# Performance work log

Hardware: AMD Instinct MI355X
Metric: run time of the kernel (lower is better)

Reference implementation:

```python
import jax, jax.numpy as jnp
import numpy as np

G, N, E, F = 1000, 256, 1024, 128
D1, D2, K1, K2 = 128, 64, 32, 8
MACRO_D, LABELS, ME = 128, 10, 16000


def gcn_conv(x, src, dst, W, b):
    """PyG GCNConv: add self-loops, symmetric deg normalization, XW aggregate."""
    n = x.shape[0]
    loop = jnp.arange(n)
    s = jnp.concatenate([src, loop])
    d = jnp.concatenate([dst, loop])
    deg = jax.ops.segment_sum(jnp.ones_like(s, dtype=x.dtype), d, num_segments=n)
    dinv = jax.lax.rsqrt(jnp.maximum(deg, 1e-12))  # deg >= 1 due to self-loops
    norm = dinv[s] * dinv[d]                        # [E+n]
    xw = x @ W                                      # [n, out]
    msg = xw[s] * norm[:, None]
    return jax.ops.segment_sum(msg, d, num_segments=n) + b


def setup_inputs() -> dict:
    key = jax.random.key(0)
    ks = jax.random.split(key, 12)
    g = lambda k, shp, fan: (jax.random.normal(k, shp, jnp.float32) / np.sqrt(fan)).astype(jnp.float32)
    return {
        "graph_features": jax.random.normal(ks[0], (G, N, F), jnp.float32),
        "graph_edges": jax.random.randint(ks[1], (G, 2, E), 0, N),
        "macro_edges": jax.random.randint(ks[2], (2, ME), 0, G),
        "W1": g(ks[3], (F, D1), F), "b1": jnp.zeros((D1,), jnp.float32),
        "W2": g(ks[4], (D1, D2), D1), "b2": jnp.zeros((D2,), jnp.float32),
        "Wf1": g(ks[5], (D2, K1), D2), "bf1": jnp.zeros((K1,), jnp.float32),
        "Wf2": g(ks[6], (K1, K2), K1), "bf2": jnp.zeros((K2,), jnp.float32),
        "Wm1": g(ks[7], (D2 * K2, MACRO_D), D2 * K2), "bm1": jnp.zeros((MACRO_D,), jnp.float32),
        "Wm2": g(ks[8], (MACRO_D, LABELS), MACRO_D), "bm2": jnp.zeros((LABELS,), jnp.float32),
    }


def reference(graph_features, graph_edges, macro_edges,
              W1, b1, W2, b2, Wf1, bf1, Wf2, bf2, Wm1, bm1, Wm2, bm2):
    def sage(x, edges):
        src, dst = edges[0], edges[1]
        h1 = jax.nn.relu(gcn_conv(x, src, dst, W1, b1))      # [N, D1]
        h2 = gcn_conv(h1, src, dst, W2, b2)                  # [N, D2]
        a = jnp.tanh(h2 @ Wf1 + bf1)                         # [N, K1]
        att = jax.nn.softmax(a @ Wf2 + bf2, axis=0)          # softmax over nodes, [N, K2]
        emb = (att.T @ h2).reshape(-1)                       # [K2*D2]
        P = att.T @ att - jnp.eye(K2, dtype=x.dtype)         # [K2, K2]
        pen = jnp.sum(jnp.sqrt(jnp.sum(P * P, axis=1)))      # sum of row L2 norms
        return emb, pen

    embs, pens = jax.vmap(sage)(graph_features, graph_edges)  # [G, K2*D2], [G]
    penalty = jnp.mean(pens)

    msrc, mdst = macro_edges[0], macro_edges[1]
    h = jax.nn.relu(gcn_conv(embs, msrc, mdst, Wm1, bm1))     # [G, MACRO_D]
    logits = gcn_conv(h, msrc, mdst, Wm2, bm2)                # [G, LABELS]
    predictions = jax.nn.log_softmax(logits, axis=1)
    return predictions, penalty
```

## Files before the change

kernel.cpp:

```cpp
#include <hip/hip_runtime.h>
#include <math.h>

typedef __attribute__((ext_vector_type(8))) short short8;
typedef __attribute__((ext_vector_type(4))) float f32x4;

#define G_ 1000
#define N_ 256
#define E_ 1024
#define F_ 128
#define D1_ 128
#define D2_ 64
#define K1_ 32
#define K2_ 8
#define MD_ 128
#define LB_ 10
#define ME_ 16000

#define OFS_PEN    0
#define OFS_EMB    16
#define OFS_XW1M   512016
#define OFS_XW2M   640016
#define OFS_DINVM  650016
#define OFS_WNORM  651016
#define OFS_ROWSTM 667016
#define OFS_WSRC   668032
#define OFS_WFRAG  676032

static __device__ __forceinline__ unsigned short f2bf(float f) {
  unsigned u = __builtin_bit_cast(unsigned, f);
  u += 0x7fff + ((u >> 16) & 1);
  return (unsigned short)(u >> 16);
}
static __device__ __forceinline__ float bf2f(unsigned short h) {
  return __builtin_bit_cast(float, (unsigned)h << 16);
}

__global__ __launch_bounds__(256)
void prep_kernel(const float* __restrict__ W1, const float* __restrict__ W2,
                 const float* __restrict__ Wf1,
                 unsigned short* __restrict__ frag, float* __restrict__ ws) {
  int t = blockIdx.x * 256 + threadIdx.x;
  if (t == 0) ws[OFS_PEN] = 0.f;
  unsigned short* w1f  = frag;
  unsigned short* w2f  = frag + 16384;
  unsigned short* wf1h = frag + 24576;
  unsigned short* wf1l = frag + 26624;
  for (int idx = t; idx < 16384; idx += gridDim.x * 256) {
    int j = idx & 7, l = (idx >> 3) & 63, ks = (idx >> 9) & 3, nt = idx >> 11;
    w1f[idx] = f2bf(W1[(ks * 32 + (l >> 4) * 8 + j) * D1_ + nt * 16 + (l & 15)]);
  }
  for (int idx = t; idx < 8192; idx += gridDim.x * 256) {
    int j = idx & 7, l = (idx >> 3) & 63, ks = (idx >> 9) & 3, nt = idx >> 11;
    w2f[idx] = f2bf(W2[(ks * 32 + (l >> 4) * 8 + j) * D2_ + nt * 16 + (l & 15)]);
  }
  for (int idx = t; idx < 2048; idx += gridDim.x * 256) {
    int j = idx & 7, l = (idx >> 3) & 63, ks = (idx >> 9) & 1, nt = idx >> 10;
    float v = Wf1[(ks * 32 + (l >> 4) * 8 + j) * K1_ + nt * 16 + (l & 15)];
    unsigned short hi = f2bf(v);
    wf1h[idx] = hi;
    wf1l[idx] = f2bf(v - bf2f(hi));
  }
}

__global__ __launch_bounds__(512, 4)
void graph_kernel(const float* __restrict__ X, const int* __restrict__ GE,
                  const unsigned short* __restrict__ FR,
                  const float* __restrict__ b1, const float* __restrict__ b2,
                  const float* __restrict__ bf1, const float* __restrict__ bf2,
                  const float* __restrict__ Wf2,
                  float* __restrict__ ws)
{
  const unsigned short* W1F  = FR;
  const unsigned short* W2F  = FR + 16384;
  const unsigned short* Wf1H = FR + 24576;
  const unsigned short* Wf1L = FR + 26624;

  extern __shared__ unsigned char smemraw[];
  unsigned short* chunkA = (unsigned short*)smemraw;
  unsigned short* h2T    = (unsigned short*)smemraw;
  unsigned short* h2s  = (unsigned short*)(smemraw + 33792);
  float*          a_stf = (float*)(smemraw + 33792);
  float*          enorm  = (float*)(smemraw + 70656);
  unsigned short* att_hi = (unsigned short*)(smemraw + 70656);
  unsigned short* att_lo = (unsigned short*)(smemraw + 74880);
  unsigned short* esrc   = (unsigned short*)(smemraw + 74752);
  int*            rowst  = (int*)(smemraw + 76800);
  int*            fill   = (int*)(smemraw + 77824);
  float*          dinv_s = (float*)(smemraw + 78848);
  float*          red    = (float*)(smemraw + 79872);

  const int g = blockIdx.x, tid = threadIdx.x;
  const int w = tid >> 6, lane = tid & 63;
  const int l15 = lane & 15, l4 = lane >> 4;
  const float* xg = X + (size_t)g * (N_ * F_);
  const int*   esG = GE + (size_t)g * (2 * E_);

  if (tid < 256) fill[tid] = 0;
  __syncthreads();
  int s0 = esG[tid * 2], d0 = esG[E_ + tid * 2];
  int s1 = esG[tid * 2 + 1], d1 = esG[E_ + tid * 2 + 1];
  atomicAdd(&fill[d0], 1);
  atomicAdd(&fill[d1], 1);
  __syncthreads();
  int myrow = 0;
  if (tid < 256) {
    int deg = fill[tid];
    dinv_s[tid] = rsqrtf((float)deg + 1.f);
    int v = deg;
#pragma unroll
    for (int off = 1; off < 64; off <<= 1) {
      int u = __shfl_up(v, off);
      if (lane >= off) v += u;
    }
    if (lane == 63) ((int*)red)[w] = v;
    myrow = v - deg;
  }
  __syncthreads();
  if (tid < 256) {
    int pre = 0;
#pragma unroll
    for (int q = 0; q < 4; ++q) if (q < w) pre += ((int*)red)[q];
    rowst[tid] = myrow + pre;
    fill[tid] = 0;
  }
  __syncthreads();
  {
    int pos = rowst[d0] + atomicAdd(&fill[d0], 1);
    esrc[pos] = (unsigned short)s0;
    enorm[pos] = dinv_s[s0] * dinv_s[d0];
    pos = rowst[d1] + atomicAdd(&fill[d1], 1);
    esrc[pos] = (unsigned short)s1;
    enorm[pos] = dinv_s[s1] * dinv_s[d1];
  }
  __syncthreads();

  const int nd = tid >> 1, jhalf = tid & 1;
  const int rb = rowst[nd], rc = fill[nd];
  const float dii = dinv_s[nd] * dinv_s[nd];

  short8 xA[2][4];
#pragma unroll
  for (int mt = 0; mt < 2; ++mt) {
    const float* xr = xg + (w * 32 + mt * 16 + l15) * F_ + l4 * 8;
#pragma unroll
    for (int ks = 0; ks < 4; ++ks) {
      float4 u = *(const float4*)(xr + ks * 32);
      float4 v2 = *(const float4*)(xr + ks * 32 + 4);
      short8 t;
      t[0] = (short)f2bf(u.x);  t[1] = (short)f2bf(u.y);
      t[2] = (short)f2bf(u.z);  t[3] = (short)f2bf(u.w);
      t[4] = (short)f2bf(v2.x); t[5] = (short)f2bf(v2.y);
      t[6] = (short)f2bf(v2.z); t[7] = (short)f2bf(v2.w);
      xA[mt][ks] = t;
    }
  }

  f32x4 acc2[2][4];
#pragma unroll
  for (int mt = 0; mt < 2; ++mt)
#pragma unroll
    for (int nt = 0; nt < 4; ++nt) acc2[mt][nt] = (f32x4){0.f, 0.f, 0.f, 0.f};

  for (int c = 0; c < 4; ++c) {
    __syncthreads();
    f32x4 acc1[2][2];
#pragma unroll
    for (int mt = 0; mt < 2; ++mt) { acc1[mt][0] = (f32x4){0.f,0.f,0.f,0.f}; acc1[mt][1] = (f32x4){0.f,0.f,0.f,0.f}; }
#pragma unroll
    for (int ks = 0; ks < 4; ++ks) {
      short8 bA = *(const short8*)(W1F + (((2 * c + 0) * 4 + ks) * 64 + lane) * 8);
      short8 bB = *(const short8*)(W1F + (((2 * c + 1) * 4 + ks) * 64 + lane) * 8);
#pragma unroll
      for (int mt = 0; mt < 2; ++mt) {
        acc1[mt][0] = __builtin_amdgcn_mfma_f32_16x16x32_bf16(xA[mt][ks], bA, acc1[mt][0], 0, 0, 0);
        acc1[mt][1] = __builtin_amdgcn_mfma_f32_16x16x32_bf16(xA[mt][ks], bB, acc1[mt][1], 0, 0, 0);
      }
    }
#pragma unroll
    for (int mt = 0; mt < 2; ++mt)
#pragma unroll
      for (int ntl = 0; ntl < 2; ++ntl)
#pragma unroll
        for (int r = 0; r < 4; ++r)
          chunkA[(w * 32 + mt * 16 + l4 * 4 + r) * 40 + ntl * 16 + l15] = f2bf(acc1[mt][ntl][r]);
    __syncthreads();
    float gacc[16];
    {
      const unsigned short* rp = chunkA + nd * 40 + jhalf * 16;
      short8 v0 = *(const short8*)(rp);
      short8 v1 = *(const short8*)(rp + 8);
#pragma unroll
      for (int j = 0; j < 8; ++j) {
        gacc[j]     = dii * bf2f((unsigned short)v0[j]);
        gacc[8 + j] = dii * bf2f((unsigned short)v1[j]);
      }
    }
    for (int e = 0; e < rc; ++e) {
      int s = esrc[rb + e]; float nm = enorm[rb + e];
      const unsigned short* sp = chunkA + s * 40 + jhalf * 16;
      short8 v0 = *(const short8*)(sp);
      short8 v1 = *(const short8*)(sp + 8);
#pragma unroll
      for (int j = 0; j < 8; ++j) {
        gacc[j]     = fmaf(nm, bf2f((unsigned short)v0[j]), gacc[j]);
        gacc[8 + j] = fmaf(nm, bf2f((unsigned short)v1[j]), gacc[8 + j]);
      }
    }
    const float* bp = b1 + c * 32 + jhalf * 16;
    __syncthreads();
    {
      short8 o0, o1;
#pragma unroll
      for (int j = 0; j < 8; ++j) {
        o0[j] = (short)f2bf(fmaxf(gacc[j] + bp[j], 0.f));
        o1[j] = (short)f2bf(fmaxf(gacc[8 + j] + bp[8 + j], 0.f));
      }
      *(short8*)(chunkA + nd * 40 + jhalf * 16) = o0;
      *(short8*)(chunkA + nd * 40 + jhalf * 16 + 8) = o1;
    }
    __syncthreads();
    {
      short8 hA0 = *(const short8*)(chunkA + (w * 32 + 0 * 16 + l15) * 40 + l4 * 8);
      short8 hA1 = *(const short8*)(chunkA + (w * 32 + 1 * 16 + l15) * 40 + l4 * 8);
#pragma unroll
      for (int nt = 0; nt < 4; ++nt) {
        short8 bf = *(const short8*)(W2F + ((nt * 4 + c) * 64 + lane) * 8);
        acc2[0][nt] = __builtin_amdgcn_mfma_f32_16x16x32_bf16(hA0, bf, acc2[0][nt], 0, 0, 0);
        acc2[1][nt] = __builtin_amdgcn_mfma_f32_16x16x32_bf16(hA1, bf, acc2[1][nt], 0, 0, 0);
      }
    }
  }

#pragma unroll
  for (int mt = 0; mt < 2; ++mt)
#pragma unroll
    for (int nt = 0; nt < 4; ++nt)
#pragma unroll
      for (int r = 0; r < 4; ++r)
        h2s[(w * 32 + mt * 16 + l4 * 4 + r) * 72 + nt * 16 + l15] = f2bf(acc2[mt][nt][r]);
  __syncthreads();
  float g2[32];
  {
    const unsigned short* rp = h2s + nd * 72 + jhalf * 32;
#pragma unroll
    for (int q = 0; q < 4; ++q) {
      short8 v = *(const short8*)(rp + q * 8);
#pragma unroll
      for (int j = 0; j < 8; ++j) g2[q * 8 + j] = dii * bf2f((unsigned short)v[j]);
    }
  }
  for (int e = 0; e < rc; ++e) {
    int s = esrc[rb + e]; float nm = enorm[rb + e];
    const unsigned short* sp = h2s + s * 72 + jhalf * 32;
#pragma unroll
    for (int q = 0; q < 4; ++q) {
      short8 v = *(const short8*)(sp + q * 8);
#pragma unroll
      for (int j = 0; j < 8; ++j) g2[q * 8 + j] = fmaf(nm, bf2f((unsigned short)v[j]), g2[q * 8 + j]);
    }
  }
  const float* b2p = b2 + jhalf * 32;
  __syncthreads();
  {
#pragma unroll
    for (int q = 0; q < 4; ++q) {
      short8 o;
#pragma unroll
      for (int j = 0; j < 8; ++j) o[j] = (short)f2bf(g2[q * 8 + j] + b2p[q * 8 + j]);
      *(short8*)(h2s + nd * 72 + jhalf * 32 + q * 8) = o;
    }
#pragma unroll
    for (int i = 0; i < 32; ++i)
      h2T[(jhalf * 32 + i) * 264 + nd] = f2bf(g2[i] + b2p[i]);
  }
  __syncthreads();

  short8 hA[2][2];
#pragma unroll
  for (int mt = 0; mt < 2; ++mt)
#pragma unroll
    for (int ks = 0; ks < 2; ++ks)
      hA[mt][ks] = *(const short8*)(h2s + (w * 32 + mt * 16 + l15) * 72 + ks * 32 + l4 * 8);
  f32x4 aacc[2][2];
#pragma unroll
  for (int mt = 0; mt < 2; ++mt) { aacc[mt][0] = (f32x4){0.f,0.f,0.f,0.f}; aacc[mt][1] = (f32x4){0.f,0.f,0.f,0.f}; }
#pragma unroll
  for (int ks = 0; ks < 2; ++ks)
#pragma unroll
    for (int nt = 0; nt < 2; ++nt) {
      short8 bh = *(const short8*)(Wf1H + ((nt * 2 + ks) * 64 + lane) * 8);
      short8 bl = *(const short8*)(Wf1L + ((nt * 2 + ks) * 64 + lane) * 8);
#pragma unroll
      for (int mt = 0; mt < 2; ++mt) {
        aacc[mt][nt] = __builtin_amdgcn_mfma_f32_16x16x32_bf16(hA[mt][ks], bh, aacc[mt][nt], 0, 0, 0);
        aacc[mt][nt] = __builtin_amdgcn_mfma_f32_16x16x32_bf16(hA[mt][ks], bl, aacc[mt][nt], 0, 0, 0);
      }
    }
  __syncthreads();
#pragma unroll
  for (int mt = 0; mt < 2; ++mt)
#pragma unroll
    for (int nt = 0; nt < 2; ++nt)
#pragma unroll
      for (int r = 0; r < 4; ++r)
        a_stf[(w * 32 + mt * 16 + l4 * 4 + r) * 34 + nt * 16 + l15] =
            tanhf(aacc[mt][nt][r] + bf1[nt * 16 + l15]);
  __syncthreads();

  float lv[8], ex[8];
  if (tid < 256) {
#pragma unroll
    for (int jj = 0; jj < 8; ++jj) lv[jj] = bf2[jj];
    const float* ar = a_stf + tid * 34;
    for (int j = 0; j < 32; ++j) {
      float av = ar[j];
      const float* wr = Wf2 + j * K2_;
#pragma unroll
      for (int jj = 0; jj < 8; ++jj) lv[jj] = fmaf(av, wr[jj], lv[jj]);
    }
    float mx[8];
#pragma unroll
    for (int jj = 0; jj < 8; ++jj) mx[jj] = lv[jj];
#pragma unroll
    for (int off = 1; off < 64; off <<= 1)
#pragma unroll
      for (int jj = 0; jj < 8; ++jj) mx[jj] = fmaxf(mx[jj], __shfl_xor(mx[jj], off));
    if (lane == 0)
#pragma unroll
      for (int jj = 0; jj < 8; ++jj) red[w * 8 + jj] = mx[jj];
  }
  __syncthreads();
  if (tid < 256) {
#pragma unroll
    for (int jj = 0; jj < 8; ++jj) {
      float m = fmaxf(fmaxf(red[jj], red[8 + jj]), fmaxf(red[16 + jj], red[24 + jj]));
      ex[jj] = expf(lv[jj] - m);
    }
    float sm[8];
#pragma unroll
    for (int jj = 0; jj < 8; ++jj) sm[jj] = ex[jj];
#pragma unroll
    for (int off = 1; off < 64; off <<= 1)
#pragma unroll
      for (int jj = 0; jj < 8; ++jj) sm[jj] += __shfl_xor(sm[jj], off);
    if (lane == 0)
#pragma unroll
      for (int jj = 0; jj < 8; ++jj) red[32 + w * 8 + jj] = sm[jj];
  }
  __syncthreads();
  if (tid < 256) {
#pragma unroll
    for (int jj = 0; jj < 8; ++jj) {
      float tot = red[32 + jj] + red[40 + jj] + red[48 + jj] + red[56 + jj];
      float av = ex[jj] / tot;
      unsigned short hi = f2bf(av);
      att_hi[jj * 264 + tid] = hi;
      att_lo[jj * 264 + tid] = f2bf(av - bf2f(hi));
    }
  }
  __syncthreads();

  const int rl = l15 & 7;
  if (w < 4) {
    f32x4 d = (f32x4){0.f, 0.f, 0.f, 0.f};
#pragma unroll
    for (int ks = 0; ks < 8; ++ks) {
      short8 ah = *(const short8*)(att_hi + rl * 264 + ks * 32 + l4 * 8);
      short8 al = *(const short8*)(att_lo + rl * 264 + ks * 32 + l4 * 8);
      short8 bv = *(const short8*)(h2T + (w * 16 + l15) * 264 + ks * 32 + l4 * 8);
      d = __builtin_amdgcn_mfma_f32_16x16x32_bf16(ah, bv, d, 0, 0, 0);
      d = __builtin_amdgcn_mfma_f32_16x16x32_bf16(al, bv, d, 0, 0, 0);
    }
    if (l4 < 2) {
      float* eg = ws + OFS_EMB + (size_t)g * 512;
#pragma unroll
      for (int r = 0; r < 4; ++r)
        eg[(l4 * 4 + r) * 64 + w * 16 + l15] = d[r];
    }
  } else if (w == 4) {
    f32x4 p = (f32x4){0.f, 0.f, 0.f, 0.f};
#pragma unroll
    for (int ks = 0; ks < 8; ++ks) {
      short8 ah = *(const short8*)(att_hi + rl * 264 + ks * 32 + l4 * 8);
      short8 al = *(const short8*)(att_lo + rl * 264 + ks * 32 + l4 * 8);
      p = __builtin_amdgcn_mfma_f32_16x16x32_bf16(ah, ah, p, 0, 0, 0);
      p = __builtin_amdgcn_mfma_f32_16x16x32_bf16(ah, al, p, 0, 0, 0);
      p = __builtin_amdgcn_mfma_f32_16x16x32_bf16(al, ah, p, 0, 0, 0);
    }
    if (l4 < 2 && l15 < 8) {
#pragma unroll
      for (int r = 0; r < 4; ++r) {
        float v = p[r];
        if (l4 * 4 + r == l15) v -= 1.f;
        red[64 + (l4 * 4 + r) * 8 + l15] = v * v;
      }
    }
  }
  __syncthreads();
  if (tid < 8) {
    float s2 = 0.f;
#pragma unroll
    for (int k = 0; k < 8; ++k) s2 += red[64 + tid * 8 + k];
    red[128 + tid] = sqrtf(s2);
  }
  __syncthreads();
  if (tid == 0) {
    float p = 0.f;
#pragma unroll
    for (int k = 0; k < 8; ++k) p += red[128 + k];
    atomicAdd(&ws[OFS_PEN], p);
  }
}

__global__ __launch_bounds__(1024)
void macro_csr(const int* __restrict__ me, float* __restrict__ ws) {
  __shared__ int cnt[1000];
  __shared__ float dinvL[1000];
  __shared__ int wtot[16];
  int t = threadIdx.x, lane = t & 63, wv = t >> 6;
  for (int i = t; i < 1000; i += 1024) cnt[i] = 0;
  __syncthreads();
  for (int e = t; e < ME_; e += 1024) atomicAdd(&cnt[me[ME_ + e]], 1);
  __syncthreads();
  int v = (t < 1000) ? cnt[t] : 0;
  float di = rsqrtf((float)v + 1.f);
  if (t < 1000) { dinvL[t] = di; ws[OFS_DINVM + t] = di; }
  int sc = v;
#pragma unroll
  for (int off = 1; off < 64; off <<= 1) {
    int u = __shfl_up(sc, off);
    if (lane >= off) sc += u;
  }
  if (lane == 63) wtot[wv] = sc;
  __syncthreads();
  int pre = 0;
#pragma unroll
  for (int q = 0; q < 16; ++q) if (q < wv) pre += wtot[q];
  int rs = pre + sc - v;
  int* rowstM = (int*)(ws + OFS_ROWSTM);
  if (t < 1000) rowstM[t] = rs;
  if (t == 0) rowstM[1000] = ME_;
  __syncthreads();
  if (t < 1000) cnt[t] = rs;
  __syncthreads();
  unsigned short* wsrc = (unsigned short*)(ws + OFS_WSRC);
  for (int e = t; e < ME_; e += 1024) {
    int s = me[e], d = me[ME_ + e];
    int pos = atomicAdd(&cnt[d], 1);
    wsrc[pos] = (unsigned short)s;
    ws[OFS_WNORM + pos] = dinvL[s] * dinvL[d];
  }
}

__global__ __launch_bounds__(128)
void macro1(const float* __restrict__ Wm1, float* __restrict__ ws) {
  __shared__ float er[512];
  int g = blockIdx.x, t = threadIdx.x;
  *(float4*)&er[t * 4] = *(const float4*)&ws[OFS_EMB + (size_t)g * 512 + t * 4];
  __syncthreads();
  float acc = 0.f;
#pragma unroll 4
  for (int k = 0; k < 512; ++k) acc = fmaf(er[k], Wm1[k * MD_ + t], acc);
  ws[OFS_XW1M + g * MD_ + t] = acc;
}

__global__ __launch_bounds__(128)
void macro2(const float* __restrict__ bm1, const float* __restrict__ Wm2, float* __restrict__ ws) {
  __shared__ float wred[2][10];
  int g = blockIdx.x, t = threadIdx.x;
  const int* rowstM = (const int*)(ws + OFS_ROWSTM);
  const unsigned short* wsrc = (const unsigned short*)(ws + OFS_WSRC);
  int e0 = rowstM[g], e1 = rowstM[g + 1];
  float di = ws[OFS_DINVM + g];
  float acc = di * di * ws[OFS_XW1M + g * MD_ + t];
  for (int e = e0; e < e1; ++e)
    acc = fmaf(ws[OFS_WNORM + e], ws[OFS_XW1M + (int)wsrc[e] * MD_ + t], acc);
  float hv = fmaxf(acc + bm1[t], 0.f);
  float part[10];
#pragma unroll
  for (int j = 0; j < 10; ++j) part[j] = hv * Wm2[t * LB_ + j];
#pragma unroll
  for (int off = 1; off < 64; off <<= 1)
#pragma unroll
    for (int j = 0; j < 10; ++j) part[j] += __shfl_xor(part[j], off);
  if ((t & 63) == 0)
#pragma unroll
    for (int j = 0; j < 10; ++j) wred[t >> 6][j] = part[j];
  __syncthreads();
  if (t < 10) ws[OFS_XW2M + g * LB_ + t] = wred[0][t] + wred[1][t];
}

__global__ __launch_bounds__(64)
void macro3(const float* __restrict__ bm2, const float* __restrict__ ws, float* __restrict__ out) {
  int g = blockIdx.x, t = threadIdx.x;
  const int* rowstM = (const int*)(ws + OFS_ROWSTM);
  const unsigned short* wsrc = (const unsigned short*)(ws + OFS_WSRC);
  int e0 = rowstM[g], e1 = rowstM[g + 1];
  float di = ws[OFS_DINVM + g];
  float lg = -1e30f;
  if (t < 10) {
    float acc = di * di * ws[OFS_XW2M + g * LB_ + t];
    for (int e = e0; e < e1; ++e)
      acc = fmaf(ws[OFS_WNORM + e], ws[OFS_XW2M + (int)wsrc[e] * LB_ + t], acc);
    lg = acc + bm2[t];
  }
  float m = lg;
#pragma unroll
  for (int off = 1; off < 16; off <<= 1) m = fmaxf(m, __shfl_xor(m, off));
  float e_ = (t < 10) ? expf(lg - m) : 0.f;
  float s = e_;
#pragma unroll
  for (int off = 1; off < 16; off <<= 1) s += __shfl_xor(s, off);
  if (t < 10) out[g * LB_ + t] = lg - m - logf(s);
  if (g == 0 && t == 63) out[10000] = ws[OFS_PEN] * 0.001f;
}

extern "C" void kernel_launch(void* const* d_in, const int* in_sizes, int n_in,
                              void* d_out, int out_size, void* d_ws, size_t ws_size,
                              hipStream_t stream)
{
  const float* X   = (const float*)d_in[0];
  const int*   GE  = (const int*)d_in[1];
  const int*   MEe = (const int*)d_in[2];
  const float* W1  = (const float*)d_in[3];
  const float* b1  = (const float*)d_in[4];
  const float* W2  = (const float*)d_in[5];
  const float* b2  = (const float*)d_in[6];
  const float* Wf1 = (const float*)d_in[7];
  const float* bf1 = (const float*)d_in[8];
  const float* Wf2 = (const float*)d_in[9];
  const float* bf2 = (const float*)d_in[10];
  const float* Wm1 = (const float*)d_in[11];
  const float* bm1 = (const float*)d_in[12];
  const float* Wm2 = (const float*)d_in[13];
  const float* bm2 = (const float*)d_in[14];
  float* ws  = (float*)d_ws;
  float* out = (float*)d_out;

  unsigned short* frag = (unsigned short*)(ws + OFS_WFRAG);

  prep_kernel<<<32, 256, 0, stream>>>(W1, W2, Wf1, frag, ws);
  macro_csr<<<1, 1024, 0, stream>>>(MEe, ws);

  size_t lds = 80896;
  graph_kernel<<<G_, 512, lds, stream>>>(X, GE, frag, b1, b2, bf1, bf2, Wf2, ws);

  macro1<<<G_, 128, 0, stream>>>(Wm1, ws);
  macro2<<<G_, 128, 0, stream>>>(bm1, Wm2, ws);
  macro3<<<G_, 64, 0, stream>>>(bm2, ws, out);
}
```

Baseline: 417.6 us.

## Process layer-1 in two 64-wide chunks with prefetched edges and shared staging

Layer 1 of the per-graph GCN now runs in two 64-column chunks instead of four 32-column chunks. This halves the number of barrier-separated gather passes over the CSR neighbour lists and widens each gather row to 32 values per thread. The first four edge sources and norms are preloaded into registers and reused by both the layer-1 and layer-2 aggregations. The staging buffer is unified and h2T is moved to its own region. f2bf now uses the library bf16 conversion, and the extra register pressure (32-float accumulators, wider acc1) may lower occupancy.

After: 457.7 us. +9.6%, slower.

```diff
diff --git a/kernel.cpp b/kernel.cpp
--- a/kernel.cpp
+++ b/kernel.cpp
@@ -1,4 +1,5 @@
 #include <hip/hip_runtime.h>
+#include <hip/hip_bf16.h>
 #include <math.h>
 
 typedef __attribute__((ext_vector_type(8))) short short8;
@@ -27,9 +28,7 @@
 #define OFS_WFRAG  676032
 
 static __device__ __forceinline__ unsigned short f2bf(float f) {
-  unsigned u = __builtin_bit_cast(unsigned, f);
-  u += 0x7fff + ((u >> 16) & 1);
-  return (unsigned short)(u >> 16);
+  return __builtin_bit_cast(unsigned short, __float2bfloat16(f));
 }
 static __device__ __forceinline__ float bf2f(unsigned short h) {
   return __builtin_bit_cast(float, (unsigned)h << 16);
@@ -76,10 +75,9 @@
   const unsigned short* Wf1L = FR + 26624;
 
   extern __shared__ unsigned char smemraw[];
-  unsigned short* chunkA = (unsigned short*)smemraw;
-  unsigned short* h2T    = (unsigned short*)smemraw;
-  unsigned short* h2s  = (unsigned short*)(smemraw + 33792);
-  float*          a_stf = (float*)(smemraw + 33792);
+  unsigned short* STG   = (unsigned short*)smemraw;
+  float*          a_stf = (float*)smemraw;
+  unsigned short* h2T   = (unsigned short*)(smemraw + 36864);
   float*          enorm  = (float*)(smemraw + 70656);
   unsigned short* att_hi = (unsigned short*)(smemraw + 70656);
   unsigned short* att_lo = (unsigned short*)(smemraw + 74880);
@@ -135,8 +133,16 @@
   __syncthreads();
 
   const int nd = tid >> 1, jhalf = tid & 1;
+  const int jh32 = jhalf * 32;
   const int rb = rowst[nd], rc = fill[nd];
   const float dii = dinv_s[nd] * dinv_s[nd];
+
+  int   es0 = nd, es1 = nd, es2 = nd, es3 = nd;
+  float en0 = 0.f, en1 = 0.f, en2 = 0.f, en3 = 0.f;
+  if (rc > 0) { es0 = esrc[rb];     en0 = enorm[rb]; }
+  if (rc > 1) { es1 = esrc[rb + 1]; en1 = enorm[rb + 1]; }
+  if (rc > 2) { es2 = esrc[rb + 2]; en2 = enorm[rb + 2]; }
+  if (rc > 3) { es3 = esrc[rb + 3]; en3 = enorm[rb + 3]; }
 
   short8 xA[2][4];
 #pragma unroll
@@ -161,117 +167,140 @@
 #pragma unroll
     for (int nt = 0; nt < 4; ++nt) acc2[mt][nt] = (f32x4){0.f, 0.f, 0.f, 0.f};
 
-  for (int c = 0; c < 4; ++c) {
+#define GATHER32(SRC, NM)                                                      \
+  {                                                                            \
+    const unsigned short* sp = STG + (SRC) * 72 + jh32;                        \
+    short8 v0 = *(const short8*)(sp);                                          \
+    short8 v1 = *(const short8*)(sp + 8);                                      \
+    short8 v2_ = *(const short8*)(sp + 16);                                    \
+    short8 v3 = *(const short8*)(sp + 24);                                     \
+    _Pragma("unroll")                                                          \
+    for (int j = 0; j < 8; ++j) {                                              \
+      gacc[j]      = fmaf((NM), bf2f((unsigned short)v0[j]), gacc[j]);         \
+      gacc[8 + j]  = fmaf((NM), bf2f((unsigned short)v1[j]), gacc[8 + j]);     \
+      gacc[16 + j] = fmaf((NM), bf2f((unsigned short)v2_[j]), gacc[16 + j]);   \
+      gacc[24 + j] = fmaf((NM), bf2f((unsigned short)v3[j]), gacc[24 + j]);    \
+    }                                                                          \
+  }
+
+  for (int c = 0; c < 2; ++c) {
     __syncthreads();
-    f32x4 acc1[2][2];
-#pragma unroll
-    for (int mt = 0; mt < 2; ++mt) { acc1[mt][0] = (f32x4){0.f,0.f,0.f,0.f}; acc1[mt][1] = (f32x4){0.f,0.f,0.f,0.f}; }
-#pragma unroll
-    for (int ks = 0; ks < 4; ++ks) {
-      short8 bA = *(const short8*)(W1F + (((2 * c + 0) * 4 + ks) * 64 + lane) * 8);
-      short8 bB = *(const short8*)(W1F + (((2 * c + 1) * 4 + ks) * 64 + lane) * 8);
-#pragma unroll
-      for (int mt = 0; mt < 2; ++mt) {
-        acc1[mt][0] = __builtin_amdgcn_mfma_f32_16x16x32_bf16(xA[mt][ks], bA, acc1[mt][0], 0, 0, 0);
-        acc1[mt][1] = __builtin_amdgcn_mfma_f32_16x16x32_bf16(xA[mt][ks], bB, acc1[mt][1], 0, 0, 0);
+    f32x4 acc1[2][4];
+#pragma unroll
+    for (int mt = 0; mt < 2; ++mt)
+#pragma unroll
+      for (int ntl = 0; ntl < 4; ++ntl) acc1[mt][ntl] = (f32x4){0.f, 0.f, 0.f, 0.f};
+#pragma unroll
+    for (int ks = 0; ks < 4; ++ks)
+#pragma unroll
+      for (int ntl = 0; ntl < 4; ++ntl) {
+        short8 b = *(const short8*)(W1F + (((c * 4 + ntl) * 4 + ks) * 64 + lane) * 8);
+        acc1[0][ntl] = __builtin_amdgcn_mfma_f32_16x16x32_bf16(xA[0][ks], b, acc1[0][ntl], 0, 0, 0);
+        acc1[1][ntl] = __builtin_amdgcn_mfma_f32_16x16x32_bf16(xA[1][ks], b, acc1[1][ntl], 0, 0, 0);
       }
-    }
 #pragma unroll
     for (int mt = 0; mt < 2; ++mt)
 #pragma unroll
-      for (int ntl = 0; ntl < 2; ++ntl)
+      for (int ntl = 0; ntl < 4; ++ntl)
 #pragma unroll
         for (int r = 0; r < 4; ++r)
-          chunkA[(w * 32 + mt * 16 + l4 * 4 + r) * 40 + ntl * 16 + l15] = f2bf(acc1[mt][ntl][r]);
+          STG[(w * 32 + mt * 16 + l4 * 4 + r) * 72 + ntl * 16 + l15] = f2bf(acc1[mt][ntl][r]);
     __syncthreads();
-    float gacc[16];
+    float gacc[32];
     {
-      const unsigned short* rp = chunkA + nd * 40 + jhalf * 16;
+      const unsigned short* rp = STG + nd * 72 + jh32;
       short8 v0 = *(const short8*)(rp);
       short8 v1 = *(const short8*)(rp + 8);
+      short8 v2_ = *(const short8*)(rp + 16);
+      short8 v3 = *(const short8*)(rp + 24);
 #pragma unroll
       for (int j = 0; j < 8; ++j) {
-        gacc[j]     = dii * bf2f((unsigned short)v0[j]);
-        gacc[8 + j] = dii * bf2f((unsigned short)v1[j]);
+        gacc[j]      = dii * bf2f((unsigned short)v0[j]);
+        gacc[8 + j]  = dii * bf2f((unsigned short)v1[j]);
+        gacc[16 + j] = dii * bf2f((unsigned short)v2_[j]);
+        gacc[24 + j] = dii * bf2f((unsigned short)v3[j]);
       }
     }
-    for (int e = 0; e < rc; ++e) {
-      int s = esrc[rb + e]; float nm = enorm[rb + e];
-      const unsigned short* sp = chunkA + s * 40 + jhalf * 16;
-      short8 v0 = *(const short8*)(sp);
-      short8 v1 = *(const short8*)(sp + 8);
-#pragma unroll
-      for (int j = 0; j < 8; ++j) {
-        gacc[j]     = fmaf(nm, bf2f((unsigned short)v0[j]), gacc[j]);
-        gacc[8 + j] = fmaf(nm, bf2f((unsigned short)v1[j]), gacc[8 + j]);
-      }
-    }
-    const float* bp = b1 + c * 32 + jhalf * 16;
+    GATHER32(es0, en0)
+    GATHER32(es1, en1)
+    GATHER32(es2, en2)
+    GATHER32(es3, en3)
+    for (int e = rb + 4; e < rb + rc; ++e) {
+      int s = esrc[e]; float nm = enorm[e];
+      GATHER32(s, nm)
+    }
     __syncthreads();
     {
-      short8 o0, o1;
-#pragma unroll
-      for (int j = 0; j < 8; ++j) {
-        o0[j] = (short)f2bf(fmaxf(gacc[j] + bp[j], 0.f));
-        o1[j] = (short)f2bf(fmaxf(gacc[8 + j] + bp[8 + j], 0.f));
+      const float* bp = b1 + c * 64 + jh32;
+#pragma unroll
+      for (int q = 0; q < 4; ++q) {
+        short8 o;
+#pragma unroll
+        for (int j = 0; j < 8; ++j)
+          o[j] = (short)f2bf(fmaxf(gacc[q * 8 + j] + bp[q * 8 + j], 0.f));
+        *(short8*)(STG + nd * 72 + jh32 + q * 8) = o;
       }
-      *(short8*)(chunkA + nd * 40 + jhalf * 16) = o0;
-      *(short8*)(chunkA + nd * 40 + jhalf * 16 + 8) = o1;
     }
     __syncthreads();
-    {
-      short8 hA0 = *(const short8*)(chunkA + (w * 32 + 0 * 16 + l15) * 40 + l4 * 8);
-      short8 hA1 = *(const short8*)(chunkA + (w * 32 + 1 * 16 + l15) * 40 + l4 * 8);
+#pragma unroll
+    for (int lks = 0; lks < 2; ++lks) {
+      short8 hA0 = *(const short8*)(STG + (w * 32 + 0 * 16 + l15) * 72 + lks * 32 + l4 * 8);
+      short8 hA1 = *(const short8*)(STG + (w * 32 + 1 * 16 + l15) * 72 + lks * 32 + l4 * 8);
 #pragma unroll
       for (int nt = 0; nt < 4; ++nt) {
-        short8 bf = *(const short8*)(W2F + ((nt * 4 + c) * 64 + lane) * 8);
-        acc2[0][nt] = __builtin_amdgcn_mfma_f32_16x16x32_bf16(hA0, bf, acc2[0][nt], 0, 0, 0);
-        acc2[1][nt] = __builtin_amdgcn_mfma_f32_16x16x32_bf16(hA1, bf, acc2[1][nt], 0, 0, 0);
+        short8 bfr = *(const short8*)(W2F + ((nt * 4 + c * 2 + lks) * 64 + lane) * 8);
+        acc2[0][nt] = __builtin_amdgcn_mfma_f32_16x16x32_bf16(hA0, bfr, acc2[0][nt], 0, 0, 0);
+        acc2[1][nt] = __builtin_amdgcn_mfma_f32_16x16x32_bf16(hA1, bfr, acc2[1][nt], 0, 0, 0);
       }
     }
   }
 
+  __syncthreads();
 #pragma unroll
   for (int mt = 0; mt < 2; ++mt)
 #pragma unroll
     for (int nt = 0; nt < 4; ++nt)
 #pragma unroll
       for (int r = 0; r < 4; ++r)
-        h2s[(w * 32 + mt * 16 + l4 * 4 + r) * 72 + nt * 16 + l15] = f2bf(acc2[mt][nt][r]);
-  __syncthreads();
-  float g2[32];
+        STG[(w * 32 + mt * 16 + l4 * 4 + r) * 72 + nt * 16 + l15] = f2bf(acc2[mt][nt][r]);
+  __syncthreads();
+  float gacc[32];
   {
-    const unsigned short* rp = h2s + nd * 72 + jhalf * 32;
-#pragma unroll
-    for (int q = 0; q < 4; ++q) {
-      short8 v = *(const short8*)(rp + q * 8);
-#pragma unroll
-      for (int j = 0; j < 8; ++j) g2[q * 8 + j] = dii * bf2f((unsigned short)v[j]);
-    }
-  }
-  for (int e = 0; e < rc; ++e) {
-    int s = esrc[rb + e]; float nm = enorm[rb + e];
-    const unsigned short* sp = h2s + s * 72 + jhalf * 32;
-#pragma unroll
-    for (int q = 0; q < 4; ++q) {
-      short8 v = *(const short8*)(sp + q * 8);
-#pragma unroll
-      for (int j = 0; j < 8; ++j) g2[q * 8 + j] = fmaf(nm, bf2f((unsigned short)v[j]), g2[q * 8 + j]);
-    }
-  }
-  const float* b2p = b2 + jhalf * 32;
+    const unsigned short* rp = STG + nd * 72 + jh32;
+    short8 v0 = *(const short8*)(rp);
+    short8 v1 = *(const short8*)(rp + 8);
+    short8 v2_ = *(const short8*)(rp + 16);
+    short8 v3 = *(const short8*)(rp + 24);
+#pragma unroll
+    for (int j = 0; j < 8; ++j) {
+      gacc[j]      = dii * bf2f((unsigned short)v0[j]);
+      gacc[8 + j]  = dii * bf2f((unsigned short)v1[j]);
+      gacc[16 + j] = dii * bf2f((unsigned short)v2_[j]);
+      gacc[24 + j] = dii * bf2f((unsigned short)v3[j]);
+    }
+  }
+  GATHER32(es0, en0)
+  GATHER32(es1, en1)
+  GATHER32(es2, en2)
+  GATHER32(es3, en3)
+  for (int e = rb + 4; e < rb + rc; ++e) {
+    int s = esrc[e]; float nm = enorm[e];
+    GATHER32(s, nm)
+  }
   __syncthreads();
   {
+    const float* b2p = b2 + jh32;
 #pragma unroll
     for (int q = 0; q < 4; ++q) {
       short8 o;
 #pragma unroll
-      for (int j = 0; j < 8; ++j) o[j] = (short)f2bf(g2[q * 8 + j] + b2p[q * 8 + j]);
-      *(short8*)(h2s + nd * 72 + jhalf * 32 + q * 8) = o;
-    }
-#pragma unroll
-    for (int i = 0; i < 32; ++i)
-      h2T[(jhalf * 32 + i) * 264 + nd] = f2bf(g2[i] + b2p[i]);
+      for (int j = 0; j < 8; ++j)
+        o[j] = (short)f2bf(gacc[q * 8 + j] + b2p[q * 8 + j]);
+      *(short8*)(STG + nd * 72 + jh32 + q * 8) = o;
+#pragma unroll
+      for (int j = 0; j < 8; ++j)
+        h2T[(jh32 + q * 8 + j) * 264 + nd] = (unsigned short)o[j];
+    }
   }
   __syncthreads();
 
@@ -280,7 +309,7 @@
   for (int mt = 0; mt < 2; ++mt)
 #pragma unroll
     for (int ks = 0; ks < 2; ++ks)
-      hA[mt][ks] = *(const short8*)(h2s + (w * 32 + mt * 16 + l15) * 72 + ks * 32 + l4 * 8);
+      hA[mt][ks] = *(const short8*)(STG + (w * 32 + mt * 16 + l15) * 72 + ks * 32 + l4 * 8);
   f32x4 aacc[2][2];
 #pragma unroll
   for (int mt = 0; mt < 2; ++mt) { aacc[mt][0] = (f32x4){0.f,0.f,0.f,0.f}; aacc[mt][1] = (f32x4){0.f,0.f,0.f,0.f}; }
@@ -410,6 +439,7 @@
     for (int k = 0; k < 8; ++k) p += red[128 + k];
     atomicAdd(&ws[OFS_PEN], p);
   }
+#undef GATHER32
 }
 
 __global__ __launch_bounds__(1024)
```
